# Kernel optimization log

Hardware: AMD Instinct MI355X
Metric: run time of the kernel (lower is better)

Reference implementation:

```python
import jax, jax.numpy as jnp
import numpy as np

D = 1024      # EMBEDDING_DIM
H = 16        # ATTENTION_HEADS
HD = 64       # HEAD_DIM
B, S = 4, 2048
EPS = 1e-5


def setup_inputs() -> dict:
    key = jax.random.key(0)
    ks = jax.random.split(key, 16)
    std = 0.02
    inp = {
        "x": jax.random.normal(ks[0], (B, S, D), dtype=jnp.float32),
        # per-head Q/K/V weights stacked: [H, D, HD]
        "Wq": jax.random.normal(ks[1], (H, D, HD), dtype=jnp.float32) * std,
        "Wk": jax.random.normal(ks[2], (H, D, HD), dtype=jnp.float32) * std,
        "Wv": jax.random.normal(ks[3], (H, D, HD), dtype=jnp.float32) * std,
        "bq": jnp.zeros((H, HD), dtype=jnp.float32),
        "bk": jnp.zeros((H, HD), dtype=jnp.float32),
        "bv": jnp.zeros((H, HD), dtype=jnp.float32),
        "Wo": jax.random.normal(ks[4], (D, D), dtype=jnp.float32) * std,
        "bo": jnp.zeros((D,), dtype=jnp.float32),
        "W1": jax.random.normal(ks[5], (D, 4 * D), dtype=jnp.float32) * std,
        "b1": jnp.zeros((4 * D,), dtype=jnp.float32),
        "W2": jax.random.normal(ks[6], (4 * D, D), dtype=jnp.float32) * std,
        "b2": jnp.zeros((D,), dtype=jnp.float32),
        # single shared LayerNorm (same module used for both pre-norms)
        "gamma": jnp.ones((D,), dtype=jnp.float32),
        "beta": jnp.zeros((D,), dtype=jnp.float32),
    }
    return inp


def _layer_norm(x, gamma, beta):
    mu = jnp.mean(x, axis=-1, keepdims=True)
    var = jnp.mean(jnp.square(x - mu), axis=-1, keepdims=True)
    return (x - mu) * jax.lax.rsqrt(var + EPS) * gamma + beta


def _block(x, Wq, Wk, Wv, bq, bk, bv, Wo, bo, W1, b1, W2, b2, gamma, beta):
    # pre-norm attention
    h = _layer_norm(x, gamma, beta)                     # [B,S,D]
    Q = jnp.einsum('bsd,hdk->bhsk', h, Wq) + bq[None, :, None, :]
    K = jnp.einsum('bsd,hdk->bhsk', h, Wk) + bk[None, :, None, :]
    V = jnp.einsum('bsd,hdk->bhsk', h, Wv) + bv[None, :, None, :]
    scores = jnp.einsum('bhsk,bhtk->bhst', Q, K) / jnp.sqrt(jnp.float32(HD))
    causal = jnp.tril(jnp.ones((S, S), dtype=bool))     # True = keep
    scores = jnp.where(causal[None, None], scores, -jnp.inf)
    attn = jax.nn.softmax(scores, axis=-1)              # [B,H,S,S]
    out = jnp.einsum('bhst,bhtk->bhsk', attn, V)        # [B,H,S,HD]
    out = out.transpose(0, 2, 1, 3).reshape(x.shape[0], x.shape[1], D)
    x = x + out @ Wo + bo
    # pre-norm MLP (shared layer norm params)
    h2 = _layer_norm(x, gamma, beta)
    mlp = jax.nn.gelu(h2 @ W1 + b1, approximate=False) @ W2 + b2
    return x + mlp


def reference(x, Wq, Wk, Wv, bq, bk, bv, Wo, bo, W1, b1, W2, b2, gamma, beta):
    return _block(x, Wq, Wk, Wv, bq, bk, bv, Wo, bo, W1, b1, W2, b2, gamma, beta)
```

## Files before the change

### kernel.cpp

```cpp
#include <hip/hip_runtime.h>
#include <hip/hip_bf16.h>

typedef __bf16  bf16x8 __attribute__((ext_vector_type(8)));
typedef float   f32x4  __attribute__((ext_vector_type(4)));
typedef short   s16x8  __attribute__((ext_vector_type(8)));

typedef const __attribute__((address_space(1))) void g_void;
typedef __attribute__((address_space(3))) void l_void;

__device__ __forceinline__ short f2b(float x) {
    __hip_bfloat16 h = __float2bfloat16(x);
    return __builtin_bit_cast(short, h);
}

__device__ __forceinline__ int pk2(float lo, float hi) {
    return (int)(unsigned short)f2b(lo) | ((int)f2b(hi) << 16);
}

__device__ __forceinline__ float fast_gelu(float v) {
    const float a = fminf(2.3022082f * (v + 0.044715f * v * v * v), 126.0f);
    const float t = exp2f(a);
    return v * t / (t + 1.0f);
}

__device__ __forceinline__ f32x4 mfma16(s16x8 a, s16x8 b, f32x4 c) {
    return __builtin_amdgcn_mfma_f32_16x16x32_bf16(
        __builtin_bit_cast(bf16x8, a), __builtin_bit_cast(bf16x8, b), c, 0, 0, 0);
}

__global__ __launch_bounds__(256) void transpose_bf16(
    const float* __restrict__ src, short* __restrict__ dst, int R, int C) {
    __shared__ float tile[32][33];
    src += (size_t)blockIdx.z * R * C;
    dst += (size_t)blockIdx.z * R * C;
    const int c0 = blockIdx.x * 32, r0 = blockIdx.y * 32;
    const int tx = threadIdx.x & 31, ty = threadIdx.x >> 5;
#pragma unroll
    for (int i = 0; i < 32; i += 8)
        tile[ty + i][tx] = src[(size_t)(r0 + ty + i) * C + c0 + tx];
    __syncthreads();
#pragma unroll
    for (int i = 0; i < 32; i += 8)
        dst[(size_t)(c0 + ty + i) * R + r0 + tx] = f2b(tile[tx][ty + i]);
}

__global__ __launch_bounds__(256) void concat_bias(
    const float* __restrict__ bq, const float* __restrict__ bk,
    const float* __restrict__ bv, float* __restrict__ o) {
    int i = blockIdx.x * 256 + threadIdx.x;
    if (i < 1024)      o[i] = bq[i];
    else if (i < 2048) o[i] = bk[i - 1024];
    else if (i < 3072) o[i] = bv[i - 2048];
}

__global__ __launch_bounds__(256) void ln_bf16(
    const float* __restrict__ x, const float* __restrict__ gamma,
    const float* __restrict__ beta, short* __restrict__ out) {
    __shared__ float red[8];
    const int row = blockIdx.x, tid = threadIdx.x;
    const float4 v = *(const float4*)(x + (size_t)row * 1024 + tid * 4);
    float s = v.x + v.y + v.z + v.w;
    float q = v.x * v.x + v.y * v.y + v.z * v.z + v.w * v.w;
#pragma unroll
    for (int off = 32; off > 0; off >>= 1) {
        s += __shfl_xor(s, off);
        q += __shfl_xor(q, off);
    }
    if ((tid & 63) == 0) { red[(tid >> 6) * 2] = s; red[(tid >> 6) * 2 + 1] = q; }
    __syncthreads();
    s = red[0] + red[2] + red[4] + red[6];
    q = red[1] + red[3] + red[5] + red[7];
    const float mu = s * (1.0f / 1024.0f);
    const float var = q * (1.0f / 1024.0f) - mu * mu;
    const float rs = rsqrtf(var + 1e-5f);
    const float4 g  = *(const float4*)(gamma + tid * 4);
    const float4 bt = *(const float4*)(beta + tid * 4);
    short4 o;
    o.x = f2b((v.x - mu) * rs * g.x + bt.x);
    o.y = f2b((v.y - mu) * rs * g.y + bt.y);
    o.z = f2b((v.z - mu) * rs * g.z + bt.z);
    o.w = f2b((v.w - mu) * rs * g.w + bt.w);
    *(short4*)(out + (size_t)row * 1024 + tid * 4) = o;
}

template <int MODE, int SWZ>
__global__ __launch_bounds__(512) void gemm_bf16(
    const short* __restrict__ A, const short* __restrict__ Bt,
    const float* __restrict__ bias, const float* __restrict__ resid,
    float* __restrict__ outf, short* __restrict__ outb, short* __restrict__ vt,
    int M, int N, int K) {
    __shared__ __align__(16) short As[2 * 128 * 32];
    __shared__ __align__(16) short Bs[2 * 128 * 32];

    const int tid = threadIdx.x;
    const int wave = tid >> 6, lane = tid & 63;
    const int l16 = lane & 15, quad = lane >> 4;
    const int wm = wave & 3, wn = wave >> 2;
    const int gx = gridDim.x;
    const int g = blockIdx.y * gx + blockIdx.x;
    const int xcd = g & 7, s = g >> 3;
    int m0, n0;
    if (SWZ == 0) {
        const int nband = gx >> 3;
        const int sm = s / nband;
        const int sn = s - sm * nband;
        m0 = sm * 128;
        n0 = (xcd * nband + sn) * 128;
    } else {
        const int mband = gridDim.y >> 3;
        const int sm = s / gx;
        m0 = (xcd * mband + sm) * 128;
        n0 = (s - sm * gx) * 128;
    }
    const int lrow = lane >> 2;
    const int lcol = (lane & 3) * 8;

    f32x4 acc[2][4] = {};

    for (int kk = 0; kk < K; kk += 64) {
#pragma unroll
        for (int p = 0; p < 2; ++p) {
            const int r = wave * 16 + lrow;
            const short* ga = A + (size_t)(m0 + r) * K + kk + p * 32 + lcol;
            short* la = &As[p * 4096 + wave * 512];
            __builtin_amdgcn_global_load_lds((g_void*)ga, (l_void*)la, 16, 0, 0);
            const short* gb = Bt + (size_t)(n0 + r) * K + kk + p * 32 + lcol;
            short* lb = &Bs[p * 4096 + wave * 512];
            __builtin_amdgcn_global_load_lds((g_void*)gb, (l_void*)lb, 16, 0, 0);
        }
        __syncthreads();
#pragma unroll
        for (int p = 0; p < 2; ++p) {
            s16x8 a[2], b[4];
#pragma unroll
            for (int t = 0; t < 2; ++t)
                a[t] = *(const s16x8*)&As[p * 4096 + (wm * 32 + t * 16 + l16) * 32 + quad * 8];
#pragma unroll
            for (int t = 0; t < 4; ++t)
                b[t] = *(const s16x8*)&Bs[p * 4096 + (wn * 64 + t * 16 + l16) * 32 + quad * 8];
#pragma unroll
            for (int mt = 0; mt < 2; ++mt)
#pragma unroll
                for (int nt = 0; nt < 4; ++nt)
                    acc[mt][nt] = mfma16(a[mt], b[nt], acc[mt][nt]);
        }
        __syncthreads();
    }

#pragma unroll
    for (int mt = 0; mt < 2; ++mt) {
#pragma unroll
        for (int nt = 0; nt < 4; ++nt) {
            const int row = m0 + wm * 32 + mt * 16 + quad * 4;
            const int col = n0 + wn * 64 + nt * 16 + l16;
            const float bc = bias[col];
            float v[4];
#pragma unroll
            for (int r = 0; r < 4; ++r) v[r] = acc[mt][nt][r] + bc;

            if (MODE == 1) {
#pragma unroll
                for (int r = 0; r < 4; ++r) {
                    const size_t rr = (size_t)(row + r);
                    outf[rr * N + col] = v[r] + resid[rr * N + col];
                }
            } else {
#pragma unroll
                for (int r = 0; r < 4; ++r)
                    outb[(size_t)(row + r) * N + col] = f2b(fast_gelu(v[r]));
            }
        }
    }
}


#define MM(MH, NH, AF, BB)                                                   \
    _Pragma("unroll") for (int p = 0; p < 2; ++p)                            \
        _Pragma("unroll") for (int ii = 0; ii < 4; ++ii)                     \
            _Pragma("unroll") for (int jj = 0; jj < 2; ++jj)                 \
                acc[(MH) * 4 + ii][(NH) * 2 + jj] =                          \
                    mfma16(AF[ii][p], BB[jj][p],                             \
                           acc[(MH) * 4 + ii][(NH) * 2 + jj]);

#define PH_MID                                                               \
    __builtin_amdgcn_s_barrier();                                            \
    __builtin_amdgcn_s_setprio(1);

#define PH_END                                                               \
    __builtin_amdgcn_s_setprio(0);                                           \
    __builtin_amdgcn_sched_barrier(0);                                       \
    __builtin_amdgcn_s_barrier();                                            \
    __builtin_amdgcn_sched_barrier(0);

#define KTILE(BUF, S1, S2, S3, S4)                                           \
    {                                                                        \
        s16x8 af[4][2], bl[2][2], bh[2][2];                                  \
                                                     \
        _Pragma("unroll") for (int ii = 0; ii < 4; ++ii)                     \
            _Pragma("unroll") for (int p = 0; p < 2; ++p)                    \
                af[ii][p] = LDA(BUF, ii, p);                                 \
        _Pragma("unroll") for (int jj = 0; jj < 2; ++jj)                     \
            _Pragma("unroll") for (int p = 0; p < 2; ++p)                    \
                bl[jj][p] = LDB(BUF, jj, p);                                 \
        S1;                                                                  \
        PH_MID;                                                              \
        MM(0, 0, af, bl);                                                    \
        PH_END;                                                              \
                                                     \
        _Pragma("unroll") for (int jj = 0; jj < 2; ++jj)                     \
            _Pragma("unroll") for (int p = 0; p < 2; ++p)                    \
                bh[jj][p] = LDB(BUF, 2 + jj, p);                             \
        S2;                                                                  \
        PH_MID;                                                              \
        MM(0, 1, af, bh);                                                    \
        PH_END;                                                              \
                                                     \
        _Pragma("unroll") for (int ii = 0; ii < 4; ++ii)                     \
            _Pragma("unroll") for (int p = 0; p < 2; ++p)                    \
                af[ii][p] = LDA(BUF, 4 + ii, p);                             \
        S3;                                                                  \
        PH_MID;                                                              \
        MM(1, 1, af, bh);                                                    \
        PH_END;                                                              \
                                      \
        S4;                                                                  \
        asm volatile("s_waitcnt vmcnt(4)" ::: "memory");                     \
        PH_MID;                                                              \
        MM(1, 0, af, bl);                                                    \
        PH_END;                                                              \
    }

template <int MODE>
__global__ __launch_bounds__(512, 2) void gemm256(
    const short* __restrict__ A, const short* __restrict__ Bt,
    const float* __restrict__ bias, const float* __restrict__ resid,
    float* __restrict__ outf, short* __restrict__ outb, short* __restrict__ vt,
    int M, int N, int K) {
    __shared__ __align__(16) short As[32768];
    __shared__ __align__(16) short Bs[32768];

    const int tid = threadIdx.x;
    const int wave = tid >> 6, lane = tid & 63;
    const int l16 = lane & 15, quad = lane >> 4;
    const int wm = wave >> 2, wn = wave & 3;

    const int nwg = gridDim.x;
    const int g = blockIdx.x;
    const int wgid = (g & 7) * (nwg >> 3) + (g >> 3);
    const int mtiles = M >> 8;
    const int m0 = (wgid % mtiles) << 8;
    const int n0 = (wgid / mtiles) << 8;

    const int rc = l16 * 32 + ((quad * 8) ^ ((l16 >> 3) << 4));
    const int a_rd = wm * 8192 + rc;
    const int b_rd = (wn >> 1) * 8192 + (wn & 1) * 4096 + rc;

    auto LDA = [&](int buf, int i, int p) {
        return *(const s16x8*)&As[buf * 16384 + a_rd + (i * 2 + p) * 512];
    };
    auto LDB = [&](int buf, int j, int p) {
        return *(const s16x8*)&Bs[buf * 16384 + b_rd + (j * 2 + p) * 512];
    };

    int r0, c0, r1, c1;
    {
        int s = tid * 16;
        int lin = s ^ (((s >> 9) & 1) << 5);
        r0 = ((lin >> 11) << 4) + ((lin >> 6) & 15);
        c0 = (((lin >> 10) & 1) << 5) + ((lin & 63) >> 1);
        s = (tid + 512) * 16;
        lin = s ^ (((s >> 9) & 1) << 5);
        r1 = ((lin >> 11) << 4) + ((lin >> 6) & 15);
        c1 = (((lin >> 10) & 1) << 5) + ((lin & 63) >> 1);
    }

    const short* gA = A + (size_t)m0 * K;
    const short* gB = Bt + (size_t)n0 * K;

    auto STAGE = [&](const short* gbase, int half, int kk, short* lds) {
        const short* s0 = gbase + (size_t)(half * 128 + r0) * K + kk + c0;
        const short* s1 = gbase + (size_t)(half * 128 + r1) * K + kk + c1;
        short* d0 = lds + half * 8192 + wave * 512;
        short* d1 = lds + half * 8192 + 4096 + wave * 512;
        __builtin_amdgcn_global_load_lds((g_void*)s0, (l_void*)d0, 16, 0, 0);
        __builtin_amdgcn_global_load_lds((g_void*)s1, (l_void*)d1, 16, 0, 0);
    };

    f32x4 acc[8][4] = {};

    STAGE(gA, 0, 0, As);
    STAGE(gA, 1, 0, As);
    STAGE(gB, 0, 0, Bs);
    STAGE(gB, 1, 0, Bs);
    STAGE(gB, 0, 64, Bs + 16384);
    STAGE(gB, 1, 64, Bs + 16384);
    asm volatile("s_waitcnt vmcnt(4)" ::: "memory");
    __builtin_amdgcn_s_barrier();
    __builtin_amdgcn_sched_barrier(0);

    const int NI = K >> 7;
    for (int it = 0; it < NI; ++it) {
        const int kA1 = (2 * it + 1) * 64;
        int kn0 = (2 * it + 2) * 64;
        if (kn0 > K - 64) kn0 = K - 64;
        int kn1 = (2 * it + 3) * 64;
        if (kn1 > K - 64) kn1 = K - 64;

        KTILE(0,
              STAGE(gA, 0, kA1, As + 16384),
              STAGE(gA, 1, kA1, As + 16384),
              STAGE(gB, 0, kn0, Bs),
              STAGE(gB, 1, kn0, Bs));
        KTILE(1,
              STAGE(gA, 0, kn0, As),
              STAGE(gA, 1, kn0, As),
              STAGE(gB, 0, kn1, Bs + 16384),
              STAGE(gB, 1, kn1, Bs + 16384));
    }

#pragma unroll
    for (int i = 0; i < 8; ++i) {
#pragma unroll
        for (int j = 0; j < 4; ++j) {
            const int row = m0 + wm * 128 + i * 16 + quad * 4;
            const int col = n0 + wn * 64 + j * 16 + l16;
            const float bc = bias[col];
            float v[4];
#pragma unroll
            for (int r = 0; r < 4; ++r) v[r] = acc[i][j][r] + bc;

            if (MODE == 0) {
                const int sel = col >> 10, within = col & 1023;
                const int h = within >> 6, hd = within & 63;
                const size_t bidx = (size_t)row >> 11, sp = row & 2047;
                if (sel == 0) {
#pragma unroll
                    for (int r = 0; r < 4; ++r) v[r] *= 0.18033688011112042f;
                }
                if (sel < 2) {
#pragma unroll
                    for (int r = 0; r < 4; ++r)
                        outb[(size_t)sel * (8192ull * 1024) +
                             ((bidx * 16 + h) * 2048 + sp + r) * 64 + hd] = f2b(v[r]);
                } else {
                    short4 o4;
                    o4.x = f2b(v[0]); o4.y = f2b(v[1]);
                    o4.z = f2b(v[2]); o4.w = f2b(v[3]);
                    *(short4*)&vt[((bidx * 16 + h) * 64 + hd) * 2048 + sp] = o4;
                }
            } else if (MODE == 1) {
#pragma unroll
                for (int r = 0; r < 4; ++r) {
                    const size_t rr = (size_t)(row + r);
                    outf[rr * N + col] = v[r] + resid[rr * N + col];
                }
            } else {
#pragma unroll
                for (int r = 0; r < 4; ++r)
                    outb[(size_t)(row + r) * N + col] = f2b(fast_gelu(v[r]));
            }
        }
    }
}

#undef KTILE
#undef PH_MID
#undef PH_END
#undef MM

__global__ __launch_bounds__(256) void attn_kernel(
    const short* __restrict__ Q, const short* __restrict__ K,
    const short* __restrict__ Vt, short* __restrict__ O) {
    const int bid = blockIdx.x;
    const int xcd = bid & 7;
    const int sub = (bid >> 3) & 7;
    const int grp = bid >> 6;
    const int bh  = grp * 8 + xcd;
    const int h = bh & 15, b = bh >> 4;
    const int gq = sub;
    const int tid = threadIdx.x, wave = tid >> 6, lane = tid & 63;
    const int l16 = lane & 15, quad = lane >> 4;

    __shared__ __align__(16) short Ks[2][64 * 72];
    __shared__ __align__(16) short Vts[2][64 * 72];
    __shared__ __align__(16) short Ps[4][16 * 72];

    const size_t bhoff = (size_t)bh * (2048ull * 64);
    const int srow = tid >> 2;
    const int sseg = (tid & 3) * 16;

    const int qts[4] = {gq, 15 - gq, 16 + gq, 31 - gq};

    for (int pass = 0; pass < 4; ++pass) {
        const int qt = qts[pass];
        const int q0 = qt * 64;
        const int q_lane = q0 + wave * 16 + l16;

        const short* qrow = Q + bhoff + (size_t)q_lane * 64;
        s16x8 bq0 = *(const s16x8*)(qrow + quad * 8);
        s16x8 bq1 = *(const s16x8*)(qrow + 32 + quad * 8);

        f32x4 oacc[4] = {};
        float lsum = 0.0f;

        s16x8 k0, k1, v0, v1;
        {
            const short* kg = K + bhoff + (size_t)srow * 64 + sseg;
            k0 = *(const s16x8*)kg;
            k1 = *(const s16x8*)(kg + 8);
            const short* vg = Vt + bhoff + (size_t)srow * 2048 + sseg;
            v0 = *(const s16x8*)vg;
            v1 = *(const s16x8*)(vg + 8);
        }

        for (int j = 0; j <= qt; ++j) {
            const int buf = j & 1;
            *(s16x8*)&Ks[buf][srow * 72 + sseg]      = k0;
            *(s16x8*)&Ks[buf][srow * 72 + sseg + 8]  = k1;
            *(s16x8*)&Vts[buf][srow * 72 + sseg]     = v0;
            *(s16x8*)&Vts[buf][srow * 72 + sseg + 8] = v1;
            __syncthreads();

            if (j < qt) {
                const short* kg = K + bhoff + (size_t)((j + 1) * 64 + srow) * 64 + sseg;
                k0 = *(const s16x8*)kg;
                k1 = *(const s16x8*)(kg + 8);
                const short* vg = Vt + bhoff + (size_t)srow * 2048 + (j + 1) * 64 + sseg;
                v0 = *(const s16x8*)vg;
                v1 = *(const s16x8*)(vg + 8);
            }

            f32x4 st[4];
#pragma unroll
            for (int s = 0; s < 4; ++s) {
                s16x8 ak0 = *(const s16x8*)&Ks[buf][(s * 16 + l16) * 72 + quad * 8];
                s16x8 ak1 = *(const s16x8*)&Ks[buf][(s * 16 + l16) * 72 + 32 + quad * 8];
                f32x4 c = {};
                c = mfma16(ak0, bq0, c);
                c = mfma16(ak1, bq1, c);
                st[s] = c;
            }
            if (j == qt) {
#pragma unroll
                for (int s = 0; s < 4; ++s)
#pragma unroll
                    for (int r = 0; r < 4; ++r) {
                        const int t = j * 64 + s * 16 + quad * 4 + r;
                        if (t > q_lane) st[s][r] = -3000.0f;
                    }
            }
            float rs = 0.0f;
#pragma unroll
            for (int s = 0; s < 4; ++s) {
#pragma unroll
                for (int r = 0; r < 4; ++r) {
                    st[s][r] = exp2f(st[s][r]);
                    rs += st[s][r];
                }
                int2 pw;
                pw.x = pk2(st[s][0], st[s][1]);
                pw.y = pk2(st[s][2], st[s][3]);
                *(int2*)&Ps[wave][l16 * 72 + s * 16 + quad * 4] = pw;
            }
            rs += __shfl_xor(rs, 16);
            rs += __shfl_xor(rs, 32);
            lsum += rs;

            asm volatile("s_waitcnt lgkmcnt(0)" ::: "memory");
            s16x8 ap0 = *(const s16x8*)&Ps[wave][l16 * 72 + quad * 8];
            s16x8 ap1 = *(const s16x8*)&Ps[wave][l16 * 72 + 32 + quad * 8];

#pragma unroll
            for (int nt = 0; nt < 4; ++nt) {
                s16x8 bv0 = *(const s16x8*)&Vts[buf][(nt * 16 + l16) * 72 + quad * 8];
                s16x8 bv1 = *(const s16x8*)&Vts[buf][(nt * 16 + l16) * 72 + 32 + quad * 8];
                oacc[nt] = mfma16(ap0, bv0, oacc[nt]);
                oacc[nt] = mfma16(ap1, bv1, oacc[nt]);
            }
        }
        __syncthreads();

        float inv[4];
#pragma unroll
        for (int r = 0; r < 4; ++r)
            inv[r] = 1.0f / __shfl(lsum, quad * 4 + r, 64);
#pragma unroll
        for (int nt = 0; nt < 4; ++nt)
#pragma unroll
            for (int r = 0; r < 4; ++r) {
                const int row = q0 + wave * 16 + quad * 4 + r;
                O[((size_t)b * 2048 + row) * 1024 + h * 64 + nt * 16 + l16] =
                    f2b(oacc[nt][r] * inv[r]);
            }
    }
}

extern "C" void kernel_launch(void* const* d_in, const int* in_sizes, int n_in,
                              void* d_out, int out_size, void* d_ws, size_t ws_size,
                              hipStream_t stream) {
    const float* x     = (const float*)d_in[0];
    const float* Wq    = (const float*)d_in[1];
    const float* Wk    = (const float*)d_in[2];
    const float* Wv    = (const float*)d_in[3];
    const float* bq    = (const float*)d_in[4];
    const float* bk    = (const float*)d_in[5];
    const float* bv    = (const float*)d_in[6];
    const float* Wo    = (const float*)d_in[7];
    const float* bo    = (const float*)d_in[8];
    const float* W1    = (const float*)d_in[9];
    const float* b1    = (const float*)d_in[10];
    const float* W2    = (const float*)d_in[11];
    const float* b2    = (const float*)d_in[12];
    const float* gamma = (const float*)d_in[13];
    const float* beta  = (const float*)d_in[14];
    float* out = (float*)d_out;

    char* ws = (char*)d_ws;
    size_t off = 0;
    auto alloc = [&](size_t bytes) -> char* {
        char* p = ws + off;
        off += (bytes + 255) & ~(size_t)255;
        return p;
    };
    short* h1    = (short*)alloc(8192ull * 1024 * 2);
    short* btqkv = (short*)alloc(3072ull * 1024 * 2);
    short* btwo  = (short*)alloc(1024ull * 1024 * 2);
    short* btw1  = (short*)alloc(4096ull * 1024 * 2);
    short* btw2  = (short*)alloc(1024ull * 4096 * 2);
    float* bqkv  = (float*)alloc(3072ull * 4);
    short* qkv   = (short*)alloc(2ull * 8192 * 1024 * 2);
    short* vt    = (short*)alloc(8192ull * 1024 * 2);
    short* aout  = (short*)alloc(8192ull * 1024 * 2);
    float* x2    = (float*)alloc(8192ull * 1024 * 4);
    short* h2    = (short*)alloc(8192ull * 1024 * 2);
    short* m1    = (short*)alloc(8192ull * 4096 * 2);

    transpose_bf16<<<dim3(2, 32, 16), 256, 0, stream>>>(Wq, btqkv, 1024, 64);
    transpose_bf16<<<dim3(2, 32, 16), 256, 0, stream>>>(Wk, btqkv + 1024ull * 1024, 1024, 64);
    transpose_bf16<<<dim3(2, 32, 16), 256, 0, stream>>>(Wv, btqkv + 2ull * 1024 * 1024, 1024, 64);
    transpose_bf16<<<dim3(32, 32, 1), 256, 0, stream>>>(Wo, btwo, 1024, 1024);
    transpose_bf16<<<dim3(128, 32, 1), 256, 0, stream>>>(W1, btw1, 1024, 4096);
    transpose_bf16<<<dim3(32, 128, 1), 256, 0, stream>>>(W2, btw2, 4096, 1024);
    concat_bias<<<12, 256, 0, stream>>>(bq, bk, bv, bqkv);

    ln_bf16<<<8192, 256, 0, stream>>>(x, gamma, beta, h1);
    gemm256<0><<<384, 512, 0, stream>>>(
        h1, btqkv, bqkv, nullptr, nullptr, qkv, vt, 8192, 3072, 1024);
    attn_kernel<<<512, 256, 0, stream>>>(
        qkv, qkv + 8192ull * 1024, vt, aout);
    gemm_bf16<1, 0><<<dim3(8, 64), 512, 0, stream>>>(
        aout, btwo, bo, x, x2, nullptr, nullptr, 8192, 1024, 1024);
    ln_bf16<<<8192, 256, 0, stream>>>(x2, gamma, beta, h2);
    gemm256<2><<<512, 512, 0, stream>>>(
        h2, btw1, b1, nullptr, nullptr, m1, nullptr, 8192, 4096, 1024);
    gemm_bf16<1, 1><<<dim3(8, 64), 512, 0, stream>>>(
        m1, btw2, b2, x2, out, nullptr, nullptr, 8192, 1024, 4096);
}
```

Before: 531.1 us.

## Reschedule GEMM prefetch stages to issue after MFMA phases with deeper lookahead

Restructures the 256x256 GEMM main loop so that global-to-LDS prefetches are issued after each MFMA phase rather than before it. The prologue is reordered and the A/B stage sequence across tiles is rotated so that loads run further ahead, with vmcnt waits adjusted to match. Explicit lgkmcnt waits and sched_barriers are added around the MFMA phases. The goal is better overlap of memory traffic with matrix work, at the risk of getting the waitcnt accounting or the LDS buffer hazards wrong.

```diff
diff --git a/kernel.cpp b/kernel.cpp
--- a/kernel.cpp
+++ b/kernel.cpp
@@ -182,12 +182,17 @@
                     mfma16(AF[ii][p], BB[jj][p],                             \
                            acc[(MH) * 4 + ii][(NH) * 2 + jj]);
 
-#define PH_MID                                                               \
+#define PH_A                                                                 \
     __builtin_amdgcn_s_barrier();                                            \
+    asm volatile("s_waitcnt lgkmcnt(0)" ::: "memory");                       \
+    __builtin_amdgcn_sched_barrier(0);                                       \
     __builtin_amdgcn_s_setprio(1);
 
-#define PH_END                                                               \
+#define PH_B                                                                 \
     __builtin_amdgcn_s_setprio(0);                                           \
+    __builtin_amdgcn_sched_barrier(0);
+
+#define PH_C                                                                 \
     __builtin_amdgcn_sched_barrier(0);                                       \
     __builtin_amdgcn_s_barrier();                                            \
     __builtin_amdgcn_sched_barrier(0);
@@ -195,39 +200,44 @@
 #define KTILE(BUF, S1, S2, S3, S4)                                           \
     {                                                                        \
         s16x8 af[4][2], bl[2][2], bh[2][2];                                  \
-                                                     \
+                                        \
         _Pragma("unroll") for (int ii = 0; ii < 4; ++ii)                     \
             _Pragma("unroll") for (int p = 0; p < 2; ++p)                    \
                 af[ii][p] = LDA(BUF, ii, p);                                 \
         _Pragma("unroll") for (int jj = 0; jj < 2; ++jj)                     \
             _Pragma("unroll") for (int p = 0; p < 2; ++p)                    \
                 bl[jj][p] = LDB(BUF, jj, p);                                 \
+        asm volatile("s_waitcnt lgkmcnt(8)" ::: "memory");                   \
+        PH_A;                                                                \
+        MM(0, 0, af, bl);                                                    \
+        PH_B;                                                                \
         S1;                                                                  \
-        PH_MID;                                                              \
-        MM(0, 0, af, bl);                                                    \
-        PH_END;                                                              \
-                                                     \
+        PH_C;                                                                \
+                                         \
         _Pragma("unroll") for (int jj = 0; jj < 2; ++jj)                     \
             _Pragma("unroll") for (int p = 0; p < 2; ++p)                    \
                 bh[jj][p] = LDB(BUF, 2 + jj, p);                             \
+        PH_A;                                                                \
+        MM(0, 1, af, bh);                                                    \
+        PH_B;                                                                \
         S2;                                                                  \
-        PH_MID;                                                              \
-        MM(0, 1, af, bh);                                                    \
-        PH_END;                                                              \
-                                                     \
+        PH_C;                                                                \
+                                         \
         _Pragma("unroll") for (int ii = 0; ii < 4; ++ii)                     \
             _Pragma("unroll") for (int p = 0; p < 2; ++p)                    \
                 af[ii][p] = LDA(BUF, 4 + ii, p);                             \
+        PH_A;                                                                \
+        MM(1, 1, af, bh);                                                    \
+        PH_B;                                                                \
         S3;                                                                  \
-        PH_MID;                                                              \
-        MM(1, 1, af, bh);                                                    \
-        PH_END;                                                              \
-                                      \
+        PH_C;                                                                \
+                          \
+        PH_A;                                                                \
+        MM(1, 0, af, bl);                                                    \
+        PH_B;                                                                \
         S4;                                                                  \
-        asm volatile("s_waitcnt vmcnt(4)" ::: "memory");                     \
-        PH_MID;                                                              \
-        MM(1, 0, af, bl);                                                    \
-        PH_END;                                                              \
+        asm volatile("s_waitcnt vmcnt(6)" ::: "memory");                     \
+        PH_C;                                                                \
     }
 
 template <int MODE>
@@ -288,35 +298,38 @@
 
     f32x4 acc[8][4] = {};
 
+    STAGE(gB, 0, 0, Bs);
+    STAGE(gB, 1, 0, Bs);
     STAGE(gA, 0, 0, As);
     STAGE(gA, 1, 0, As);
-    STAGE(gB, 0, 0, Bs);
-    STAGE(gB, 1, 0, Bs);
+    asm volatile("s_waitcnt vmcnt(4)" ::: "memory");
     STAGE(gB, 0, 64, Bs + 16384);
     STAGE(gB, 1, 64, Bs + 16384);
-    asm volatile("s_waitcnt vmcnt(4)" ::: "memory");
+    STAGE(gA, 0, 64, As + 16384);
+    asm volatile("s_waitcnt vmcnt(6)" ::: "memory");
     __builtin_amdgcn_s_barrier();
     __builtin_amdgcn_sched_barrier(0);
 
     const int NI = K >> 7;
     for (int it = 0; it < NI; ++it) {
-        const int kA1 = (2 * it + 1) * 64;
-        int kn0 = (2 * it + 2) * 64;
-        if (kn0 > K - 64) kn0 = K - 64;
-        int kn1 = (2 * it + 3) * 64;
-        if (kn1 > K - 64) kn1 = K - 64;
+        const int kT1 = (2 * it + 1) * 64;
+        int kT2 = (2 * it + 2) * 64;
+        if (kT2 > K - 64) kT2 = K - 64;
+        int kT3 = (2 * it + 3) * 64;
+        if (kT3 > K - 64) kT3 = K - 64;
 
         KTILE(0,
-              STAGE(gA, 0, kA1, As + 16384),
-              STAGE(gA, 1, kA1, As + 16384),
-              STAGE(gB, 0, kn0, Bs),
-              STAGE(gB, 1, kn0, Bs));
+              STAGE(gA, 1, kT1, As + 16384),
+              STAGE(gB, 0, kT2, Bs),
+              STAGE(gB, 1, kT2, Bs),
+              STAGE(gA, 0, kT2, As));
         KTILE(1,
-              STAGE(gA, 0, kn0, As),
-              STAGE(gA, 1, kn0, As),
-              STAGE(gB, 0, kn1, Bs + 16384),
-              STAGE(gB, 1, kn1, Bs + 16384));
-    }
+              STAGE(gA, 1, kT2, As),
+              STAGE(gB, 0, kT3, Bs + 16384),
+              STAGE(gB, 1, kT3, Bs + 16384),
+              STAGE(gA, 0, kT3, As + 16384));
+    }
+    asm volatile("s_waitcnt vmcnt(0)" ::: "memory");
 
 #pragma unroll
     for (int i = 0; i < 8; ++i) {
@@ -364,8 +377,9 @@
 }
 
 #undef KTILE
-#undef PH_MID
-#undef PH_END
+#undef PH_A
+#undef PH_B
+#undef PH_C
 #undef MM
 
 __global__ __launch_bounds__(256) void attn_kernel(
```

After: 531.0 us. Within noise of the previous version (-0.0%).
